# Kernel tuning notes

Measured on AMD Instinct MI355X. Metric: run time of the kernel, lower is better.

Reference implementation:

```python
import jax, jax.numpy as jnp
import numpy as np

N_NODES = 10000
N_EDGES = 320000
F = 128
N_RBF = 20


def setup_inputs() -> dict:
    key = jax.random.key(0)
    ks = jax.random.split(key, 12)
    inp = {
        "idx_i": jax.random.randint(ks[0], (N_EDGES,), 0, N_NODES),
        "idx_j": jax.random.randint(ks[1], (N_EDGES,), 0, N_NODES),
        "rel_dir": jax.random.normal(ks[2], (N_EDGES, 3), dtype=jnp.float32),
        "rel_dist_cut": jax.random.uniform(ks[3], (N_EDGES,), dtype=jnp.float32),
        "rbf_features": jax.random.normal(ks[4], (N_EDGES, N_RBF), dtype=jnp.float32),
        "scalar_features": jax.random.normal(ks[5], (N_NODES, F), dtype=jnp.float32),
        "vector_features": jax.random.normal(ks[6], (N_NODES, F, 3), dtype=jnp.float32),
        # learned params: scalar_network = Linear(F,F) -> SiLU -> Linear(F,3F); rbf_network = Linear(N_RBF,3F)
        "W1": jax.random.normal(ks[7], (F, F), dtype=jnp.float32) / np.sqrt(F),
        "b1": jnp.zeros((F,), dtype=jnp.float32),
        "W2": jax.random.normal(ks[8], (F, 3 * F), dtype=jnp.float32) / np.sqrt(F),
        "b2": jnp.zeros((3 * F,), dtype=jnp.float32),
        "Wr": jax.random.normal(ks[9], (N_RBF, 3 * F), dtype=jnp.float32) / np.sqrt(N_RBF),
        "br": jnp.zeros((3 * F,), dtype=jnp.float32),
    }
    return inp


def reference(idx_i, idx_j, rel_dir, rel_dist_cut, rbf_features,
              scalar_features, vector_features, W1, b1, W2, b2, Wr, br):
    num_nodes, num_features = scalar_features.shape
    # per-node MLP: [N, 3F]
    phi = jax.nn.silu(scalar_features @ W1 + b1) @ W2 + b2
    # distance gate: [E, 3F]
    Wg = (rbf_features @ Wr + br) * rel_dist_cut[:, None]
    # gather neighbor phi and gate
    phi_W = phi[idx_j] * Wg                       # [E, 3F]
    phi_W_vv = phi_W[:, :num_features]            # [E, F]
    phi_W_ss = phi_W[:, num_features:2 * num_features]
    phi_W_vs = phi_W[:, 2 * num_features:]
    # per-receiver edge counts (bincount)
    counts = jax.ops.segment_sum(jnp.ones((idx_i.shape[0],), phi_W.dtype),
                                 idx_i, num_segments=num_nodes)  # [N]
    scalar_residuals = jax.ops.segment_sum(phi_W_ss, idx_i, num_segments=num_nodes)
    scalar_residuals = scalar_residuals / counts[:, None]
    # per-edge vector message: [E, F, 3]
    v_edge = (vector_features[idx_j] * phi_W_vv[:, :, None]
              + phi_W_vs[:, :, None] * rel_dir[:, None, :])
    vector_residuals = jax.ops.segment_sum(v_edge, idx_i, num_segments=num_nodes)
    vector_residuals = vector_residuals / counts[:, None, None]
    return (scalar_features + scalar_residuals,
            vector_features + vector_residuals)
```

## Files before the change

### kernel.cpp

```cpp
#include <hip/hip_runtime.h>
#include <hip/hip_bf16.h>

#define NN 10000
#define NE 320000
#define FDIM 128
#define NRBF 20
#define PHI_DIM 384
#define NKEY NN
#define SCAN_BLOCKS 40

typedef unsigned int uint;
typedef unsigned short ushort;

#if __has_builtin(__builtin_amdgcn_fdot2_f32_bf16)
#define USE_DOT2 1
typedef __bf16 bf16x2 __attribute__((ext_vector_type(2)));
#else
#define USE_DOT2 0
#endif

__device__ __forceinline__ ushort f2bf(float x) {
  __hip_bfloat16 b = __float2bfloat16(x);
  return *(ushort*)&b;
}
__device__ __forceinline__ float bflo(uint u) { return __uint_as_float(u << 16); }
__device__ __forceinline__ float bfhi(uint u) { return __uint_as_float(u & 0xffff0000u); }


__global__ void phi_kernel(const float* __restrict__ S, const float* __restrict__ W1,
                           const float* __restrict__ b1, const float* __restrict__ W2,
                           const float* __restrict__ b2, const float* __restrict__ vf,
                           const int* __restrict__ idx_i, int* __restrict__ counts,
                           char* __restrict__ tab) {
  __shared__ float s_s[4][FDIM];
  __shared__ float h_s[4][FDIM];
  const int t = threadIdx.x;
  const int n0 = blockIdx.x * 4;
  atomicAdd(&counts[idx_i[blockIdx.x * 128 + t]], 1);
#pragma unroll
  for (int n = 0; n < 4; n++) s_s[n][t] = S[(n0 + n) * FDIM + t];
  __syncthreads();
  float acc[4];
#pragma unroll
  for (int n = 0; n < 4; n++) acc[n] = 0.f;
  for (int k = 0; k < FDIM; k++) {
    float w = W1[k * FDIM + t];
#pragma unroll
    for (int n = 0; n < 4; n++) acc[n] += s_s[n][k] * w;
  }
  float bb = b1[t];
#pragma unroll
  for (int n = 0; n < 4; n++) {
    float x = acc[n] + bb;
    h_s[n][t] = x / (1.0f + expf(-x));
  }
  __syncthreads();
  float a0[4], a1[4], a2[4];
#pragma unroll
  for (int n = 0; n < 4; n++) { a0[n] = 0.f; a1[n] = 0.f; a2[n] = 0.f; }
  for (int k = 0; k < FDIM; k++) {
    float w0 = W2[k * PHI_DIM + t];
    float w1 = W2[k * PHI_DIM + t + 128];
    float w2 = W2[k * PHI_DIM + t + 256];
#pragma unroll
    for (int n = 0; n < 4; n++) {
      float hv = h_s[n][k];
      a0[n] += hv * w0;
      a1[n] += hv * w1;
      a2[n] += hv * w2;
    }
  }
  float c0 = b2[t], c1 = b2[t + 128], c2 = b2[t + 256];
#pragma unroll
  for (int n = 0; n < 4; n++) {
    const int node = n0 + n;
    const float p0 = a0[n] + c0;
    const float p1 = a1[n] + c1;
    const float p2 = a2[n] + c2;
    const float* src = vf + (size_t)node * (FDIM * 3) + t * 3;
    const uint wx = f2bf(src[0] * p0);
    const uint wy = f2bf(src[1] * p0);
    const uint wz = f2bf(src[2] * p0);
    char* pb = tab + (size_t)node * 1280;
    ((uint*)pb)[t] = (wy << 16) | wx;
    ((uint*)(pb + 512))[t] = ((uint)f2bf(p1) << 16) | wz;
    ((ushort*)(pb + 1024))[t] = f2bf(p2);
  }
}

__global__ void scan1_kernel(const int* __restrict__ counts, int* __restrict__ offsets,
                             int* __restrict__ blocksums) {
  __shared__ int s[256];
  const int t = threadIdx.x;
  const int idx = blockIdx.x * 256 + t;
  const int c = counts[idx];
  s[t] = c;
  __syncthreads();
  for (int off = 1; off < 256; off <<= 1) {
    int v = (t >= off) ? s[t - off] : 0;
    __syncthreads();
    s[t] += v;
    __syncthreads();
  }
  if (idx < NKEY) offsets[idx] = s[t] - c;
  if (t == 255) blocksums[blockIdx.x] = s[255];
}

__global__ void scan2_kernel(int* __restrict__ blocksums, int* __restrict__ offsets) {
  __shared__ int s[64];
  const int t = threadIdx.x;
  int v0 = (t < SCAN_BLOCKS) ? blocksums[t] : 0;
  s[t] = v0;
  __syncthreads();
  for (int off = 1; off < 64; off <<= 1) {
    int v = (t >= off) ? s[t - off] : 0;
    __syncthreads();
    s[t] += v;
    __syncthreads();
  }
  if (t < SCAN_BLOCKS) blocksums[t] = s[t] - v0;
  if (t == SCAN_BLOCKS - 1) offsets[NKEY] = s[t];
}

__global__ void scan3_kernel(int* __restrict__ offsets, const int* __restrict__ blocksums) {
  const int idx = blockIdx.x * 256 + threadIdx.x;
  if (idx < NKEY) offsets[idx] += blocksums[blockIdx.x];
}

__global__ void stage_kernel(const int* __restrict__ idx_i, const int* __restrict__ idx_j,
                             const float* __restrict__ cut, const float* __restrict__ dir,
                             const float* __restrict__ rbf, const int* __restrict__ offsets,
                             int* __restrict__ counts, uint* __restrict__ edata,
                             int* __restrict__ jlist) {
  int e = blockIdx.x * blockDim.x + threadIdx.x;
  if (e >= NE) return;
  int i = idx_i[e];
  int pos = atomicSub(&counts[i], 1) - 1;
  const int slot = offsets[i] + pos;
  jlist[slot] = idx_j[e];
  const float c = cut[e];
  uint w[12];
  w[0] = ((uint)f2bf(dir[e * 3 + 1]) << 16) | f2bf(dir[e * 3 + 0]);
  const float* rb = rbf + (size_t)e * NRBF;
#pragma unroll
  for (int r = 0; r < 10; r++) {
    uint lo = (uint)f2bf(rb[2 * r] * c);
    uint hi = (uint)f2bf(rb[2 * r + 1] * c);
    w[1 + r] = (hi << 16) | lo;
  }
  w[11] = ((uint)f2bf(dir[e * 3 + 2]) << 16) | f2bf(c);
  uint4* d = (uint4*)(edata + (size_t)slot * 12);
  d[0] = make_uint4(w[0], w[1], w[2], w[3]);
  d[1] = make_uint4(w[4], w[5], w[6], w[7]);
  d[2] = make_uint4(w[8], w[9], w[10], w[11]);
}

__global__ __launch_bounds__(128, 5) void node_kernel(
    const uint* __restrict__ edata, const int* __restrict__ jlist,
    const float* __restrict__ Wr, const float* __restrict__ br,
    const char* __restrict__ tab, const float* __restrict__ sf,
    const float* __restrict__ vf, const int* __restrict__ offsets,
    float* __restrict__ out) {
  const int f = threadIdx.x;
#if USE_DOT2
  bf16x2 wrA[11], wrB[11], wrC[11];
#pragma unroll
  for (int r = 0; r < 10; r++) {
    uint a = ((uint)f2bf(Wr[(2 * r + 1) * PHI_DIM + f]) << 16) | f2bf(Wr[(2 * r) * PHI_DIM + f]);
    uint b = ((uint)f2bf(Wr[(2 * r + 1) * PHI_DIM + f + 128]) << 16) |
             f2bf(Wr[(2 * r) * PHI_DIM + f + 128]);
    uint c = ((uint)f2bf(Wr[(2 * r + 1) * PHI_DIM + f + 256]) << 16) |
             f2bf(Wr[(2 * r) * PHI_DIM + f + 256]);
    wrA[r] = __builtin_bit_cast(bf16x2, a);
    wrB[r] = __builtin_bit_cast(bf16x2, b);
    wrC[r] = __builtin_bit_cast(bf16x2, c);
  }
  wrA[10] = __builtin_bit_cast(bf16x2, (uint)f2bf(br[f]));
  wrB[10] = __builtin_bit_cast(bf16x2, (uint)f2bf(br[f + 128]));
  wrC[10] = __builtin_bit_cast(bf16x2, (uint)f2bf(br[f + 256]));
#else
  float wrA[22], wrB[22], wrC[22];
#pragma unroll
  for (int r = 0; r < NRBF; r++) {
    wrA[r] = Wr[r * PHI_DIM + f];
    wrB[r] = Wr[r * PHI_DIM + f + 128];
    wrC[r] = Wr[r * PHI_DIM + f + 256];
  }
  wrA[20] = br[f];      wrA[21] = 0.f;
  wrB[20] = br[f + 128]; wrB[21] = 0.f;
  wrC[20] = br[f + 256]; wrC[21] = 0.f;
#endif
  const int n = blockIdx.x;
  const int beg = offsets[n], end = offsets[n + 1];
  float ss = 0.f, ax = 0.f, ay = 0.f, az = 0.f;
  const int f4 = f * 4;

  auto process = [&](uint4 e0, uint4 e1, uint4 e2, uint d0, uint d1, uint zu) {
    uint rbp[11] = {e0.y, e0.z, e0.w, e1.x, e1.y, e1.z, e1.w, e2.x, e2.y, e2.z, e2.w};
    const float dx = bflo(e0.x);
    const float dy = bfhi(e0.x);
    const float dz = bfhi(rbp[10]);
    float g0 = 0.f, g1 = 0.f, g2 = 0.f;
#if USE_DOT2
#pragma unroll
    for (int r = 0; r < 11; r++) {
      bf16x2 rp = __builtin_bit_cast(bf16x2, rbp[r]);
      g0 = __builtin_amdgcn_fdot2_f32_bf16(rp, wrA[r], g0, false);
      g1 = __builtin_amdgcn_fdot2_f32_bf16(rp, wrB[r], g1, false);
      g2 = __builtin_amdgcn_fdot2_f32_bf16(rp, wrC[r], g2, false);
    }
#else
#pragma unroll
    for (int r = 0; r < 11; r++) {
      float rlo = bflo(rbp[r]);
      float rhi = bfhi(rbp[r]);
      g0 += rlo * wrA[2 * r] + rhi * wrA[2 * r + 1];
      g1 += rlo * wrB[2 * r] + rhi * wrB[2 * r + 1];
      g2 += rlo * wrC[2 * r] + rhi * wrC[2 * r + 1];
    }
#endif
    const float vs = bflo(zu) * g2;
    ss += bfhi(d1) * g1;
    ax += bflo(d0) * g0 + vs * dx;
    ay += bfhi(d0) * g0 + vs * dy;
    az += bflo(d1) * g0 + vs * dz;
  };

  int p = beg;
  for (; p + 4 <= end; p += 4) {
    const int j0 = jlist[p], j1 = jlist[p + 1], j2 = jlist[p + 2], j3 = jlist[p + 3];
    const char* B0 = tab + (size_t)j0 * 1280;
    const char* B1 = tab + (size_t)j1 * 1280;
    const char* B2 = tab + (size_t)j2 * 1280;
    const char* B3 = tab + (size_t)j3 * 1280;
    const uint d00 = *(const uint*)(B0 + f4), d01 = *(const uint*)(B0 + 512 + f4);
    const uint z0 = *(const ushort*)(B0 + 1024 + f * 2);
    const uint d10 = *(const uint*)(B1 + f4), d11 = *(const uint*)(B1 + 512 + f4);
    const uint z1 = *(const ushort*)(B1 + 1024 + f * 2);
    const uint d20 = *(const uint*)(B2 + f4), d21 = *(const uint*)(B2 + 512 + f4);
    const uint z2 = *(const ushort*)(B2 + 1024 + f * 2);
    const uint d30 = *(const uint*)(B3 + f4), d31 = *(const uint*)(B3 + 512 + f4);
    const uint z3 = *(const ushort*)(B3 + 1024 + f * 2);
    {
      const uint4* r0 = (const uint4*)(edata + (size_t)p * 12);
      const uint4* r1 = (const uint4*)(edata + (size_t)(p + 1) * 12);
      uint4 a0 = r0[0], a1 = r0[1], a2 = r0[2];
      uint4 b0 = r1[0], b1 = r1[1], b2 = r1[2];
      process(a0, a1, a2, d00, d01, z0);
      process(b0, b1, b2, d10, d11, z1);
    }
    {
      const uint4* r2 = (const uint4*)(edata + (size_t)(p + 2) * 12);
      const uint4* r3 = (const uint4*)(edata + (size_t)(p + 3) * 12);
      uint4 a0 = r2[0], a1 = r2[1], a2 = r2[2];
      uint4 b0 = r3[0], b1 = r3[1], b2 = r3[2];
      process(a0, a1, a2, d20, d21, z2);
      process(b0, b1, b2, d30, d31, z3);
    }
  }
  for (; p < end; p++) {
    const int j0 = jlist[p];
    const char* B0 = tab + (size_t)j0 * 1280;
    const uint d00 = *(const uint*)(B0 + f4), d01 = *(const uint*)(B0 + 512 + f4);
    const uint z0 = *(const ushort*)(B0 + 1024 + f * 2);
    const uint4* r0 = (const uint4*)(edata + (size_t)p * 12);
    process(r0[0], r0[1], r0[2], d00, d01, z0);
  }

  const float inv = 1.0f / (float)(end - beg);
  out[(size_t)n * FDIM + f] = sf[(size_t)n * FDIM + f] + ss * inv;
  float* ov = out + (size_t)NN * FDIM + (size_t)n * (FDIM * 3) + f * 3;
  const float* iv = vf + (size_t)n * (FDIM * 3) + f * 3;
  ov[0] = iv[0] + ax * inv;
  ov[1] = iv[1] + ay * inv;
  ov[2] = iv[2] + az * inv;
}

extern "C" void kernel_launch(void* const* d_in, const int* in_sizes, int n_in,
                              void* d_out, int out_size, void* d_ws, size_t ws_size,
                              hipStream_t stream) {
  const int* idx_i = (const int*)d_in[0];
  const int* idx_j = (const int*)d_in[1];
  const float* rel_dir = (const float*)d_in[2];
  const float* cut = (const float*)d_in[3];
  const float* rbf = (const float*)d_in[4];
  const float* sf = (const float*)d_in[5];
  const float* vf = (const float*)d_in[6];
  const float* W1 = (const float*)d_in[7];
  const float* b1 = (const float*)d_in[8];
  const float* W2 = (const float*)d_in[9];
  const float* b2 = (const float*)d_in[10];
  const float* Wr = (const float*)d_in[11];
  const float* br = (const float*)d_in[12];
  float* out = (float*)d_out;

  char* w = (char*)d_ws;
  int* counts = (int*)w;
  int* offsets = (int*)(w + 40960);
  int* blocksums = (int*)(w + 81920);
  uint* edata = (uint*)(w + 90112);
  char* tab = w + 15450112;
  int* jlist = (int*)(w + 28250112);

  hipMemsetAsync(w, 0, 40960, stream);
  hipLaunchKernelGGL(phi_kernel, dim3(NN / 4), dim3(128), 0, stream, sf, W1, b1, W2, b2, vf,
                     idx_i, counts, tab);
  hipLaunchKernelGGL(scan1_kernel, dim3(SCAN_BLOCKS), dim3(256), 0, stream, counts, offsets,
                     blocksums);
  hipLaunchKernelGGL(scan2_kernel, dim3(1), dim3(64), 0, stream, blocksums, offsets);
  hipLaunchKernelGGL(scan3_kernel, dim3(SCAN_BLOCKS), dim3(256), 0, stream, offsets, blocksums);
  hipLaunchKernelGGL(stage_kernel, dim3((NE + 255) / 256), dim3(256), 0, stream, idx_i, idx_j,
                     cut, rel_dir, rbf, offsets, counts, edata, jlist);
  hipLaunchKernelGGL(node_kernel, dim3(NN), dim3(128), 0, stream, edata, jlist, Wr, br, tab, sf,
                     vf, offsets, out);
}
```

Before: 170.4 us.

## Batch 16 nodes per phi block, fold scan fixup into consumers, shrink gather unroll

The phi MLP kernel now processes 16 nodes per block instead of 4, so each W1/W2 weight load is reused across more nodes; each thread also does 4 count atomics. The third scan pass is removed, and the stage and node kernels add the block prefix sum inline when reading offsets. The node kernel's edge loop is unrolled by 2 instead of 4, which lowers register pressure but leaves fewer gathers in flight. Phi now launches only 625 blocks and holds many accumulators in registers, which may hurt occupancy and latency hiding in that kernel.

```diff
diff --git a/kernel.cpp b/kernel.cpp
--- a/kernel.cpp
+++ b/kernel.cpp
@@ -32,38 +32,42 @@
                            const float* __restrict__ b2, const float* __restrict__ vf,
                            const int* __restrict__ idx_i, int* __restrict__ counts,
                            char* __restrict__ tab) {
-  __shared__ float s_s[4][FDIM];
-  __shared__ float h_s[4][FDIM];
+  __shared__ float s_s[16][FDIM];
+  __shared__ float h_s[16][FDIM];
   const int t = threadIdx.x;
-  const int n0 = blockIdx.x * 4;
-  atomicAdd(&counts[idx_i[blockIdx.x * 128 + t]], 1);
-#pragma unroll
-  for (int n = 0; n < 4; n++) s_s[n][t] = S[(n0 + n) * FDIM + t];
+  const int n0 = blockIdx.x * 16;
+  {
+    const int e0 = (blockIdx.x * 128 + t) * 4;
+#pragma unroll
+    for (int q = 0; q < 4; q++) atomicAdd(&counts[idx_i[e0 + q]], 1);
+  }
+#pragma unroll
+  for (int n = 0; n < 16; n++) s_s[n][t] = S[(n0 + n) * FDIM + t];
   __syncthreads();
-  float acc[4];
-#pragma unroll
-  for (int n = 0; n < 4; n++) acc[n] = 0.f;
+  float acc[16];
+#pragma unroll
+  for (int n = 0; n < 16; n++) acc[n] = 0.f;
   for (int k = 0; k < FDIM; k++) {
     float w = W1[k * FDIM + t];
 #pragma unroll
-    for (int n = 0; n < 4; n++) acc[n] += s_s[n][k] * w;
+    for (int n = 0; n < 16; n++) acc[n] += s_s[n][k] * w;
   }
   float bb = b1[t];
 #pragma unroll
-  for (int n = 0; n < 4; n++) {
+  for (int n = 0; n < 16; n++) {
     float x = acc[n] + bb;
     h_s[n][t] = x / (1.0f + expf(-x));
   }
   __syncthreads();
-  float a0[4], a1[4], a2[4];
-#pragma unroll
-  for (int n = 0; n < 4; n++) { a0[n] = 0.f; a1[n] = 0.f; a2[n] = 0.f; }
+  float a0[16], a1[16], a2[16];
+#pragma unroll
+  for (int n = 0; n < 16; n++) { a0[n] = 0.f; a1[n] = 0.f; a2[n] = 0.f; }
   for (int k = 0; k < FDIM; k++) {
     float w0 = W2[k * PHI_DIM + t];
     float w1 = W2[k * PHI_DIM + t + 128];
     float w2 = W2[k * PHI_DIM + t + 256];
 #pragma unroll
-    for (int n = 0; n < 4; n++) {
+    for (int n = 0; n < 16; n++) {
       float hv = h_s[n][k];
       a0[n] += hv * w0;
       a1[n] += hv * w1;
@@ -72,7 +76,7 @@
   }
   float c0 = b2[t], c1 = b2[t + 128], c2 = b2[t + 256];
 #pragma unroll
-  for (int n = 0; n < 4; n++) {
+  for (int n = 0; n < 16; n++) {
     const int node = n0 + n;
     const float p0 = a0[n] + c0;
     const float p1 = a1[n] + c1;
@@ -122,21 +126,16 @@
   if (t == SCAN_BLOCKS - 1) offsets[NKEY] = s[t];
 }
 
-__global__ void scan3_kernel(int* __restrict__ offsets, const int* __restrict__ blocksums) {
-  const int idx = blockIdx.x * 256 + threadIdx.x;
-  if (idx < NKEY) offsets[idx] += blocksums[blockIdx.x];
-}
-
 __global__ void stage_kernel(const int* __restrict__ idx_i, const int* __restrict__ idx_j,
                              const float* __restrict__ cut, const float* __restrict__ dir,
                              const float* __restrict__ rbf, const int* __restrict__ offsets,
-                             int* __restrict__ counts, uint* __restrict__ edata,
-                             int* __restrict__ jlist) {
+                             const int* __restrict__ blocksums, int* __restrict__ counts,
+                             uint* __restrict__ edata, int* __restrict__ jlist) {
   int e = blockIdx.x * blockDim.x + threadIdx.x;
   if (e >= NE) return;
   int i = idx_i[e];
   int pos = atomicSub(&counts[i], 1) - 1;
-  const int slot = offsets[i] + pos;
+  const int slot = offsets[i] + blocksums[i >> 8] + pos;
   jlist[slot] = idx_j[e];
   const float c = cut[e];
   uint w[12];
@@ -160,7 +159,7 @@
     const float* __restrict__ Wr, const float* __restrict__ br,
     const char* __restrict__ tab, const float* __restrict__ sf,
     const float* __restrict__ vf, const int* __restrict__ offsets,
-    float* __restrict__ out) {
+    const int* __restrict__ blocksums, float* __restrict__ out) {
   const int f = threadIdx.x;
 #if USE_DOT2
   bf16x2 wrA[11], wrB[11], wrC[11];
@@ -186,12 +185,13 @@
     wrB[r] = Wr[r * PHI_DIM + f + 128];
     wrC[r] = Wr[r * PHI_DIM + f + 256];
   }
-  wrA[20] = br[f];      wrA[21] = 0.f;
+  wrA[20] = br[f];       wrA[21] = 0.f;
   wrB[20] = br[f + 128]; wrB[21] = 0.f;
   wrC[20] = br[f + 256]; wrC[21] = 0.f;
 #endif
   const int n = blockIdx.x;
-  const int beg = offsets[n], end = offsets[n + 1];
+  const int beg = offsets[n] + blocksums[n >> 8];
+  const int end = (n + 1 < NKEY) ? (offsets[n + 1] + blocksums[(n + 1) >> 8]) : offsets[NKEY];
   float ss = 0.f, ax = 0.f, ay = 0.f, az = 0.f;
   const int f4 = f * 4;
 
@@ -227,38 +227,23 @@
   };
 
   int p = beg;
-  for (; p + 4 <= end; p += 4) {
-    const int j0 = jlist[p], j1 = jlist[p + 1], j2 = jlist[p + 2], j3 = jlist[p + 3];
+  for (; p + 2 <= end; p += 2) {
+    const int j0 = jlist[p];
+    const int j1 = jlist[p + 1];
     const char* B0 = tab + (size_t)j0 * 1280;
     const char* B1 = tab + (size_t)j1 * 1280;
-    const char* B2 = tab + (size_t)j2 * 1280;
-    const char* B3 = tab + (size_t)j3 * 1280;
     const uint d00 = *(const uint*)(B0 + f4), d01 = *(const uint*)(B0 + 512 + f4);
     const uint z0 = *(const ushort*)(B0 + 1024 + f * 2);
     const uint d10 = *(const uint*)(B1 + f4), d11 = *(const uint*)(B1 + 512 + f4);
     const uint z1 = *(const ushort*)(B1 + 1024 + f * 2);
-    const uint d20 = *(const uint*)(B2 + f4), d21 = *(const uint*)(B2 + 512 + f4);
-    const uint z2 = *(const ushort*)(B2 + 1024 + f * 2);
-    const uint d30 = *(const uint*)(B3 + f4), d31 = *(const uint*)(B3 + 512 + f4);
-    const uint z3 = *(const ushort*)(B3 + 1024 + f * 2);
-    {
-      const uint4* r0 = (const uint4*)(edata + (size_t)p * 12);
-      const uint4* r1 = (const uint4*)(edata + (size_t)(p + 1) * 12);
-      uint4 a0 = r0[0], a1 = r0[1], a2 = r0[2];
-      uint4 b0 = r1[0], b1 = r1[1], b2 = r1[2];
-      process(a0, a1, a2, d00, d01, z0);
-      process(b0, b1, b2, d10, d11, z1);
-    }
-    {
-      const uint4* r2 = (const uint4*)(edata + (size_t)(p + 2) * 12);
-      const uint4* r3 = (const uint4*)(edata + (size_t)(p + 3) * 12);
-      uint4 a0 = r2[0], a1 = r2[1], a2 = r2[2];
-      uint4 b0 = r3[0], b1 = r3[1], b2 = r3[2];
-      process(a0, a1, a2, d20, d21, z2);
-      process(b0, b1, b2, d30, d31, z3);
-    }
-  }
-  for (; p < end; p++) {
+    const uint4* r0 = (const uint4*)(edata + (size_t)p * 12);
+    const uint4* r1 = (const uint4*)(edata + (size_t)(p + 1) * 12);
+    uint4 a0 = r0[0], a1 = r0[1], a2 = r0[2];
+    uint4 b0 = r1[0], b1 = r1[1], b2 = r1[2];
+    process(a0, a1, a2, d00, d01, z0);
+    process(b0, b1, b2, d10, d11, z1);
+  }
+  if (p < end) {
     const int j0 = jlist[p];
     const char* B0 = tab + (size_t)j0 * 1280;
     const uint d00 = *(const uint*)(B0 + f4), d01 = *(const uint*)(B0 + 512 + f4);
@@ -303,14 +288,13 @@
   int* jlist = (int*)(w + 28250112);
 
   hipMemsetAsync(w, 0, 40960, stream);
-  hipLaunchKernelGGL(phi_kernel, dim3(NN / 4), dim3(128), 0, stream, sf, W1, b1, W2, b2, vf,
+  hipLaunchKernelGGL(phi_kernel, dim3(NN / 16), dim3(128), 0, stream, sf, W1, b1, W2, b2, vf,
                      idx_i, counts, tab);
   hipLaunchKernelGGL(scan1_kernel, dim3(SCAN_BLOCKS), dim3(256), 0, stream, counts, offsets,
                      blocksums);
   hipLaunchKernelGGL(scan2_kernel, dim3(1), dim3(64), 0, stream, blocksums, offsets);
-  hipLaunchKernelGGL(scan3_kernel, dim3(SCAN_BLOCKS), dim3(256), 0, stream, offsets, blocksums);
   hipLaunchKernelGGL(stage_kernel, dim3((NE + 255) / 256), dim3(256), 0, stream, idx_i, idx_j,
-                     cut, rel_dir, rbf, offsets, counts, edata, jlist);
+                     cut, rel_dir, rbf, offsets, blocksums, counts, edata, jlist);
   hipLaunchKernelGGL(node_kernel, dim3(NN), dim3(128), 0, stream, edata, jlist, Wr, br, tab, sf,
-                     vf, offsets, out);
-}
+                     vf, offsets, blocksums, out);
+}
```

Measured after the change: 194.1 us. +13.9%, slower.
